# Kernel tuning notes

Measured on AMD Instinct MI355X. Metric: run time of the kernel, lower is better.

The kernel has to match this reference:

```python
import jax, jax.numpy as jnp
import numpy as np

B = 1024
N = 100  # graph_size
D = 128


def setup_inputs() -> dict:
    key = jax.random.key(0)
    k1, k2 = jax.random.split(key)
    x = jax.random.normal(k1, (B * N, D), dtype=jnp.float32)
    edge_index = jax.random.randint(k2, (2, B * N * (N - 1)), 0, N, dtype=jnp.int64)
    return {"x": x, "edge_index": edge_index, "graph_size": N}


def reference(x, edge_index, graph_size):
    # x: [B*N, D] -> [B, N, D]; edge_index is split but never used in the math.
    b = x.shape[0] // graph_size
    xb = x.reshape(b, graph_size, -1)
    # per-graph dot-product logits: [B, N, N]
    logits = jnp.einsum('bnd,bmd->bnm', xb, xb)
    # segment softmax with index j = column index of the flattened [N*N] logits:
    # normalizes over rows i for each column j -> softmax along axis=1.
    return jax.nn.softmax(logits, axis=1)
```

## Files before the change

### kernel.cpp

```cpp
#include <hip/hip_runtime.h>

#define NG 100
#define DD 128
#define NPAD 112
#define LSTRIDE 136

typedef __attribute__((ext_vector_type(8))) short bf16x8;
typedef __attribute__((ext_vector_type(4))) float floatx4;

__device__ __forceinline__ float red_max16(float v) {
    v = fmaxf(v, __shfl_xor(v, 1, 64));
    v = fmaxf(v, __shfl_xor(v, 2, 64));
    v = fmaxf(v, __shfl_xor(v, 4, 64));
    v = fmaxf(v, __shfl_xor(v, 8, 64));
    return v;
}
__device__ __forceinline__ float red_sum16(float v) {
    v += __shfl_xor(v, 1, 64);
    v += __shfl_xor(v, 2, 64);
    v += __shfl_xor(v, 4, 64);
    v += __shfl_xor(v, 8, 64);
    return v;
}

__global__ __launch_bounds__(256, 4)
void dotdec_mfma(const float* __restrict__ x, float* __restrict__ out) {
    __shared__ unsigned short xs[NPAD * LSTRIDE];
    const int t    = threadIdx.x;
    const int lane = t & 63;
    const int wave = t >> 6;
    const int quad = lane >> 4;
    const int lr   = lane & 15;
    const size_t b = blockIdx.x;
    const float* xb = x   + b * (size_t)(NG * DD);
    float*       ob = out + b * (size_t)(NG * NG);

    if (t < 192) {
        int r = 100 + (t >> 4), c = t & 15;
        *(uint4*)&xs[r * LSTRIDE + c * 8] = make_uint4(0u, 0u, 0u, 0u);
    }
#pragma unroll
    for (int k = 0; k < 7; ++k) {
        int p = t + 256 * k;
        if (p < NG * 16) {
            int n = p >> 4, gp = p & 15;
            float4 v0 = ((const float4*)xb)[n * 32 + gp * 2];
            float4 v1 = ((const float4*)xb)[n * 32 + gp * 2 + 1];
            unsigned int u0 = (__float_as_uint(v0.x) >> 16) | (__float_as_uint(v0.y) & 0xffff0000u);
            unsigned int u1 = (__float_as_uint(v0.z) >> 16) | (__float_as_uint(v0.w) & 0xffff0000u);
            unsigned int u2 = (__float_as_uint(v1.x) >> 16) | (__float_as_uint(v1.y) & 0xffff0000u);
            unsigned int u3 = (__float_as_uint(v1.z) >> 16) | (__float_as_uint(v1.w) & 0xffff0000u);
            *(uint4*)&xs[n * LSTRIDE + gp * 8] = make_uint4(u0, u1, u2, u3);
        }
    }
    __syncthreads();

    const int c0 = wave;
    const int c1 = (wave < 3) ? wave + 4 : wave;
    floatx4 acc0[7], acc1[7];
#pragma unroll
    for (int r = 0; r < 7; ++r) {
        acc0[r] = (floatx4){0.f, 0.f, 0.f, 0.f};
        acc1[r] = (floatx4){0.f, 0.f, 0.f, 0.f};
    }
#pragma unroll
    for (int k = 0; k < 4; ++k) {
        const int koff = k * 32 + quad * 8;
        bf16x8 a0 = *(const bf16x8*)&xs[(c0 * 16 + lr) * LSTRIDE + koff];
        bf16x8 a1 = *(const bf16x8*)&xs[(c1 * 16 + lr) * LSTRIDE + koff];
#pragma unroll
        for (int r = 0; r < 7; ++r) {
            bf16x8 bb = *(const bf16x8*)&xs[(r * 16 + lr) * LSTRIDE + koff];
            acc0[r] = __builtin_amdgcn_mfma_f32_16x16x32_bf16(a0, bb, acc0[r], 0, 0, 0);
            acc1[r] = __builtin_amdgcn_mfma_f32_16x16x32_bf16(a1, bb, acc1[r], 0, 0, 0);
        }
    }

    floatx4 mx0 = acc0[0], mx1 = acc1[0];
#pragma unroll
    for (int r = 1; r < 7; ++r)
#pragma unroll
        for (int j = 0; j < 4; ++j) {
            mx0[j] = fmaxf(mx0[j], acc0[r][j]);
            mx1[j] = fmaxf(mx1[j], acc1[r][j]);
        }
#pragma unroll
    for (int j = 0; j < 4; ++j) {
        mx0[j] = red_max16(mx0[j]);
        mx1[j] = red_max16(mx1[j]);
    }

    floatx4 s0 = (floatx4){0.f, 0.f, 0.f, 0.f};
    floatx4 s1 = (floatx4){0.f, 0.f, 0.f, 0.f};
#pragma unroll
    for (int r = 0; r < 7; ++r)
#pragma unroll
        for (int j = 0; j < 4; ++j) {
            float e0 = __expf(acc0[r][j] - mx0[j]); acc0[r][j] = e0; s0[j] += e0;
            float e1 = __expf(acc1[r][j] - mx1[j]); acc1[r][j] = e1; s1[j] += e1;
        }
    floatx4 inv0, inv1;
#pragma unroll
    for (int j = 0; j < 4; ++j) {
        inv0[j] = __builtin_amdgcn_rcpf(red_sum16(s0[j]));
        inv1[j] = __builtin_amdgcn_rcpf(red_sum16(s1[j]));
    }

    const bool dual = (wave < 3) && !(c1 == 6 && quad != 0);
    const int mo0 = c0 * 16 + quad * 4;
    const int mo1 = c1 * 16 + quad * 4;
#pragma unroll
    for (int r = 0; r < 7; ++r) {
        int n = r * 16 + lr;
        if (n < NG) {
            floatx4 o0 = acc0[r] * inv0;
            *(floatx4*)&ob[n * NG + mo0] = o0;
            if (dual) {
                floatx4 o1 = acc1[r] * inv1;
                *(floatx4*)&ob[n * NG + mo1] = o1;
            }
        }
    }
}

extern "C" void kernel_launch(void* const* d_in, const int* in_sizes, int n_in,
                              void* d_out, int out_size, void* d_ws, size_t ws_size,
                              hipStream_t stream) {
    const float* x = (const float*)d_in[0];
    float* out = (float*)d_out;
    const int B = in_sizes[0] / (NG * DD);
    hipLaunchKernelGGL(dotdec_mfma, dim3(B), dim3(256), 0, stream, x, out);
}
```

Baseline: 160.0 us.

## Use seven waves with swapped MFMA operands and stage output through LDS

Each of seven waves now owns one 16-column tile. The MFMA operands are swapped so each lane holds whole columns, which replaces the 16-lane shuffle reductions with a few intra-register ops plus two cross-quad shuffles. Normalized results are staged in a 40 KB shared buffer that reuses the input staging area, then written to global memory as fully contiguous float4 stores. This adds two block barriers and a larger LDS footprint, which may limit occupancy relative to the launch bound of 7.

```diff
diff --git a/kernel.cpp b/kernel.cpp
--- a/kernel.cpp
+++ b/kernel.cpp
@@ -8,24 +8,12 @@
 typedef __attribute__((ext_vector_type(8))) short bf16x8;
 typedef __attribute__((ext_vector_type(4))) float floatx4;
 
-__device__ __forceinline__ float red_max16(float v) {
-    v = fmaxf(v, __shfl_xor(v, 1, 64));
-    v = fmaxf(v, __shfl_xor(v, 2, 64));
-    v = fmaxf(v, __shfl_xor(v, 4, 64));
-    v = fmaxf(v, __shfl_xor(v, 8, 64));
-    return v;
-}
-__device__ __forceinline__ float red_sum16(float v) {
-    v += __shfl_xor(v, 1, 64);
-    v += __shfl_xor(v, 2, 64);
-    v += __shfl_xor(v, 4, 64);
-    v += __shfl_xor(v, 8, 64);
-    return v;
-}
+__global__ __launch_bounds__(448, 7)
+void dotdec_mfma(const float* __restrict__ x, float* __restrict__ out) {
+    __shared__ __align__(16) char smraw[NG * NG * 4];
+    unsigned short* xs = (unsigned short*)smraw;
+    float*          fo = (float*)smraw;
 
-__global__ __launch_bounds__(256, 4)
-void dotdec_mfma(const float* __restrict__ x, float* __restrict__ out) {
-    __shared__ unsigned short xs[NPAD * LSTRIDE];
     const int t    = threadIdx.x;
     const int lane = t & 63;
     const int wave = t >> 6;
@@ -40,8 +28,8 @@
         *(uint4*)&xs[r * LSTRIDE + c * 8] = make_uint4(0u, 0u, 0u, 0u);
     }
 #pragma unroll
-    for (int k = 0; k < 7; ++k) {
-        int p = t + 256 * k;
+    for (int k = 0; k < 4; ++k) {
+        int p = t + 448 * k;
         if (p < NG * 16) {
             int n = p >> 4, gp = p & 15;
             float4 v0 = ((const float4*)xb)[n * 32 + gp * 2];
@@ -55,71 +43,62 @@
     }
     __syncthreads();
 
-    const int c0 = wave;
-    const int c1 = (wave < 3) ? wave + 4 : wave;
-    floatx4 acc0[7], acc1[7];
+    floatx4 acc[7];
 #pragma unroll
-    for (int r = 0; r < 7; ++r) {
-        acc0[r] = (floatx4){0.f, 0.f, 0.f, 0.f};
-        acc1[r] = (floatx4){0.f, 0.f, 0.f, 0.f};
-    }
+    for (int r = 0; r < 7; ++r) acc[r] = (floatx4){0.f, 0.f, 0.f, 0.f};
 #pragma unroll
     for (int k = 0; k < 4; ++k) {
         const int koff = k * 32 + quad * 8;
-        bf16x8 a0 = *(const bf16x8*)&xs[(c0 * 16 + lr) * LSTRIDE + koff];
-        bf16x8 a1 = *(const bf16x8*)&xs[(c1 * 16 + lr) * LSTRIDE + koff];
+        bf16x8 bb = *(const bf16x8*)&xs[(wave * 16 + lr) * LSTRIDE + koff];
 #pragma unroll
         for (int r = 0; r < 7; ++r) {
-            bf16x8 bb = *(const bf16x8*)&xs[(r * 16 + lr) * LSTRIDE + koff];
-            acc0[r] = __builtin_amdgcn_mfma_f32_16x16x32_bf16(a0, bb, acc0[r], 0, 0, 0);
-            acc1[r] = __builtin_amdgcn_mfma_f32_16x16x32_bf16(a1, bb, acc1[r], 0, 0, 0);
+            bf16x8 aa = *(const bf16x8*)&xs[(r * 16 + lr) * LSTRIDE + koff];
+            acc[r] = __builtin_amdgcn_mfma_f32_16x16x32_bf16(aa, bb, acc[r], 0, 0, 0);
         }
     }
 
-    floatx4 mx0 = acc0[0], mx1 = acc1[0];
+    floatx4 mx4 = acc[0];
 #pragma unroll
     for (int r = 1; r < 7; ++r)
 #pragma unroll
-        for (int j = 0; j < 4; ++j) {
-            mx0[j] = fmaxf(mx0[j], acc0[r][j]);
-            mx1[j] = fmaxf(mx1[j], acc1[r][j]);
-        }
-#pragma unroll
-    for (int j = 0; j < 4; ++j) {
-        mx0[j] = red_max16(mx0[j]);
-        mx1[j] = red_max16(mx1[j]);
-    }
+        for (int i = 0; i < 4; ++i) mx4[i] = fmaxf(mx4[i], acc[r][i]);
+    float mx = fmaxf(fmaxf(mx4[0], mx4[1]), fmaxf(mx4[2], mx4[3]));
+    mx = fmaxf(mx, __shfl_xor(mx, 16, 64));
+    mx = fmaxf(mx, __shfl_xor(mx, 32, 64));
 
-    floatx4 s0 = (floatx4){0.f, 0.f, 0.f, 0.f};
-    floatx4 s1 = (floatx4){0.f, 0.f, 0.f, 0.f};
+    floatx4 s4 = (floatx4){0.f, 0.f, 0.f, 0.f};
 #pragma unroll
     for (int r = 0; r < 7; ++r)
 #pragma unroll
-        for (int j = 0; j < 4; ++j) {
-            float e0 = __expf(acc0[r][j] - mx0[j]); acc0[r][j] = e0; s0[j] += e0;
-            float e1 = __expf(acc1[r][j] - mx1[j]); acc1[r][j] = e1; s1[j] += e1;
+        for (int i = 0; i < 4; ++i) {
+            float e = __expf(acc[r][i] - mx);
+            acc[r][i] = e;
+            s4[i] += e;
         }
-    floatx4 inv0, inv1;
+    float s = (s4[0] + s4[1]) + (s4[2] + s4[3]);
+    s += __shfl_xor(s, 16, 64);
+    s += __shfl_xor(s, 32, 64);
+    const float inv = __builtin_amdgcn_rcpf(s);
+
+    __syncthreads();
+
+    const int m = wave * 16 + lr;
+    if (m < NG) {
 #pragma unroll
-    for (int j = 0; j < 4; ++j) {
-        inv0[j] = __builtin_amdgcn_rcpf(red_sum16(s0[j]));
-        inv1[j] = __builtin_amdgcn_rcpf(red_sum16(s1[j]));
+        for (int r = 0; r < 7; ++r)
+#pragma unroll
+            for (int i = 0; i < 4; ++i) {
+                int n = r * 16 + quad * 4 + i;
+                if (n < NG) fo[n * NG + m] = acc[r][i] * inv;
+            }
     }
+    __syncthreads();
 
-    const bool dual = (wave < 3) && !(c1 == 6 && quad != 0);
-    const int mo0 = c0 * 16 + quad * 4;
-    const int mo1 = c1 * 16 + quad * 4;
 #pragma unroll
-    for (int r = 0; r < 7; ++r) {
-        int n = r * 16 + lr;
-        if (n < NG) {
-            floatx4 o0 = acc0[r] * inv0;
-            *(floatx4*)&ob[n * NG + mo0] = o0;
-            if (dual) {
-                floatx4 o1 = acc1[r] * inv1;
-                *(floatx4*)&ob[n * NG + mo1] = o1;
-            }
-        }
+    for (int k = 0; k < 6; ++k) {
+        int f = t + 448 * k;
+        if (f < (NG * NG) / 4)
+            ((float4*)ob)[f] = *(const float4*)&fo[f * 4];
     }
 }
 
@@ -129,5 +108,5 @@
     const float* x = (const float*)d_in[0];
     float* out = (float*)d_out;
     const int B = in_sizes[0] / (NG * DD);
-    hipLaunchKernelGGL(dotdec_mfma, dim3(B), dim3(256), 0, stream, x, out);
+    hipLaunchKernelGGL(dotdec_mfma, dim3(B), dim3(448), 0, stream, x, out);
 }
```

Measured after the change: 158.0 us. No clear change (-1.2%).
